# Optimization experiments

Hardware: AMD Instinct MI355X
Metric: run time of the kernel (lower is better)

The kernel has to match this reference:

```python
import jax, jax.numpy as jnp
import numpy as np

NB, D, ED, N, K, DTR = 4, 1024, 2048, 32, 4, 64
B, L = 1, 1024


def setup_inputs():
    key = jax.random.key(0)
    ks = jax.random.split(key, 10)
    g = lambda k, s, sc=0.02: jax.random.normal(k, s, dtype=jnp.float32) * sc
    A_log = jnp.log(jnp.broadcast_to(jnp.arange(1, N + 1, dtype=jnp.float32), (NB, ED, N))) + 0.0
    return {
        "x": g(ks[0], (B, L, D), 1.0),
        "Wi": g(ks[1], (D, D)),
        "bi": jnp.zeros((D,), jnp.float32),
        "ln_g": jnp.ones((NB, D), jnp.float32),
        "ln_b": jnp.zeros((NB, D), jnp.float32),
        "in_w": g(ks[2], (NB, 2 * ED, D)),
        "conv_w": g(ks[3], (NB, ED, 1, K), 0.2),
        "conv_b": jnp.zeros((NB, ED), jnp.float32),
        "xproj_w": g(ks[4], (NB, DTR + 2 * N, ED)),
        "dtproj_w": g(ks[5], (NB, ED, DTR), 0.1),
        "dtproj_b": jnp.full((NB, ED), -4.0, jnp.float32),
        "A_log": A_log,
        "Dp": jnp.ones((NB, ED), jnp.float32),
        "out_w": g(ks[6], (NB, D, ED)),
        "fn_g": jnp.ones((D,), jnp.float32),
        "fn_b": jnp.zeros((D,), jnp.float32),
        "sp_w": g(ks[7], (N, D)),
        "sp_b": jnp.zeros((N,), jnp.float32),
    }


def layernorm(x, g, b, eps=1e-5):
    m = jnp.mean(x, axis=-1, keepdims=True)
    v = jnp.mean(jnp.square(x - m), axis=-1, keepdims=True)
    return (x - m) * jax.lax.rsqrt(v + eps) * g + b


def mamba(u_in, in_w, conv_w, conv_b, xproj_w, dtproj_w, dtproj_b, A_log, Dp, out_w):
    # u_in: (B, L, D)
    xz = u_in @ in_w.T                       # (B, L, 2*ED)
    u, z = jnp.split(xz, 2, axis=-1)         # each (B, L, ED)
    # causal depthwise conv over time
    uc = jnp.swapaxes(u, 1, 2)               # (B, ED, L)
    uc = jax.lax.conv_general_dilated(uc, conv_w, (1,), [(K - 1, 0)], feature_group_count=ED)
    uc = uc + conv_b[None, :, None]
    u = jax.nn.silu(jnp.swapaxes(uc, 1, 2))  # (B, L, ED)
    x_dbl = u @ xproj_w.T                    # (B, L, DTR + 2N)
    dt, Bm, Cm = jnp.split(x_dbl, [DTR, DTR + N], axis=-1)
    delta = jax.nn.softplus(dt @ dtproj_w.T + dtproj_b)  # (B, L, ED)
    A = -jnp.exp(A_log)                                  # (ED, N)
    dA = jnp.exp(delta[..., None] * A)                   # (B, L, ED, N)
    dBu = (delta * u)[..., None] * Bm[:, :, None, :]     # (B, L, ED, N)

    def step(h, inp):
        dA_t, dBu_t, C_t = inp
        h = dA_t * h + dBu_t
        y = jnp.einsum('ben,bn->be', h, C_t)
        return h, y

    h0 = jnp.zeros((u.shape[0], ED, N), u.dtype)
    _, ys = jax.lax.scan(step, h0, (jnp.swapaxes(dA, 0, 1), jnp.swapaxes(dBu, 0, 1), jnp.swapaxes(Cm, 0, 1)))
    y = jnp.swapaxes(ys, 0, 1) + u * Dp      # (B, L, ED)
    y = y * jax.nn.silu(z)
    return y @ out_w.T                       # (B, L, D)


def reference(x, Wi, bi, ln_g, ln_b, in_w, conv_w, conv_b, xproj_w, dtproj_w, dtproj_b, A_log, Dp, out_w, fn_g, fn_b, sp_w, sp_b):
    h = x @ Wi.T + bi
    for i in range(NB):
        normed = layernorm(h, ln_g[i], ln_b[i])
        h = h + mamba(normed, in_w[i], conv_w[i], conv_b[i], xproj_w[i],
                      dtproj_w[i], dtproj_b[i], A_log[i], Dp[i], out_w[i])
    h = layernorm(h, fn_g, fn_b)
    state = jnp.mean(h, axis=1) @ sp_w.T + sp_b   # (B, N)
    return h, state
```

## Files before the change

### kernel.cpp

```cpp
#include <hip/hip_runtime.h>
#include <math.h>

#define D_    1024
#define ED_   2048
#define NST   32
#define KCONV 4
#define DTR_  64
#define L_    1024
#define NB_   4
#define NCH   8
#define CHUNK (L_ / NCH)
#define ZSPL  4
#define XPZ   16

typedef __bf16 bf16_8 __attribute__((ext_vector_type(8)));
typedef __bf16 bf16_4 __attribute__((ext_vector_type(4)));
typedef float  f32x4  __attribute__((ext_vector_type(4)));

__device__ __forceinline__ float softplus_f(float x) {
  return x > 20.f ? x : log1pf(expf(x));
}
__device__ __forceinline__ float silu_f(float x) {
  return x / (1.f + expf(-x));
}

__global__ __launch_bounds__(256) void f2bf_k(
    const float* __restrict__ in, __bf16* __restrict__ out, int n)
{
  const int i = (blockIdx.x * 256 + threadIdx.x) * 8;
  if (i >= n) return;
  const float4 a = *reinterpret_cast<const float4*>(in + i);
  const float4 b = *reinterpret_cast<const float4*>(in + i + 4);
  bf16_8 v;
  v[0]=(__bf16)a.x; v[1]=(__bf16)a.y; v[2]=(__bf16)a.z; v[3]=(__bf16)a.w;
  v[4]=(__bf16)b.x; v[5]=(__bf16)b.y; v[6]=(__bf16)b.z; v[7]=(__bf16)b.w;
  *reinterpret_cast<bf16_8*>(out + i) = v;
}

__global__ __launch_bounds__(256) void gemm_mfma(
    const __bf16* __restrict__ A, int lda,
    const __bf16* __restrict__ W, int ldw,
    const float* __restrict__ bias, float* __restrict__ C, int ldc,
    int K, int flags)
{
  __shared__ __bf16 As[128 * 64];
  __shared__ __bf16 Ws[128 * 64];
  const int tid  = threadIdx.x;
  const int lane = tid & 63;
  const int w    = tid >> 6;
  const int wr   = w >> 1, wc = w & 1;
  const int row0 = blockIdx.y * 128, col0 = blockIdx.x * 128;

  f32x4 acc[4][4] = {};

  for (int k0 = 0; k0 < K; k0 += 64) {
    #pragma unroll
    for (int j = 0; j < 4; ++j) {
      const int inst = w * 4 + j;
      const int row  = inst * 8 + (lane >> 3);
      const int lu   = (lane & 7) ^ (row & 7);
      __builtin_amdgcn_global_load_lds(
          (const __attribute__((address_space(1))) void*)(A + (size_t)(row0 + row) * lda + k0 + lu * 8),
          (__attribute__((address_space(3))) void*)(&As[inst * 512]), 16, 0, 0);
      __builtin_amdgcn_global_load_lds(
          (const __attribute__((address_space(1))) void*)(W + (size_t)(col0 + row) * ldw + k0 + lu * 8),
          (__attribute__((address_space(3))) void*)(&Ws[inst * 512]), 16, 0, 0);
    }
    __syncthreads();
    const int r16 = lane & 15;
    const int uq  = lane >> 4;
    #pragma unroll
    for (int ks = 0; ks < 2; ++ks) {
      bf16_8 af[4], bfr[4];
      #pragma unroll
      for (int m = 0; m < 4; ++m) {
        const int row = wr * 64 + m * 16 + r16;
        const int pu  = (ks * 4 + uq) ^ (row & 7);
        af[m] = *reinterpret_cast<const bf16_8*>(&As[row * 64 + pu * 8]);
      }
      #pragma unroll
      for (int n = 0; n < 4; ++n) {
        const int row = wc * 64 + n * 16 + r16;
        const int pu  = (ks * 4 + uq) ^ (row & 7);
        bfr[n] = *reinterpret_cast<const bf16_8*>(&Ws[row * 64 + pu * 8]);
      }
      #pragma unroll
      for (int m = 0; m < 4; ++m)
        #pragma unroll
        for (int n = 0; n < 4; ++n)
          acc[m][n] = __builtin_amdgcn_mfma_f32_16x16x32_bf16(af[m], bfr[n], acc[m][n], 0, 0, 0);
    }
    __syncthreads();
  }

  const int crow = (lane >> 4) * 4;
  const int ccol = lane & 15;
  #pragma unroll
  for (int m = 0; m < 4; ++m)
    #pragma unroll
    for (int n = 0; n < 4; ++n) {
      const int col = col0 + wc * 64 + n * 16 + ccol;
      const float bv = (flags & 4) ? bias[col] : 0.f;
      #pragma unroll
      for (int r = 0; r < 4; ++r) {
        const int row = row0 + wr * 64 + m * 16 + crow + r;
        float* cp = C + (size_t)row * ldc + col;
        float v = acc[m][n][r] + bv;
        if (flags & 2) v = softplus_f(v);
        if (flags & 1) v += *cp;
        *cp = v;
      }
    }
}

__global__ __launch_bounds__(256) void gemm_mfma_sk(
    const __bf16* __restrict__ A, const __bf16* __restrict__ W,
    float* __restrict__ partials, int M, int N, int K, int Kc)
{
  __shared__ __bf16 As[128 * 64];
  __shared__ __bf16 Ws[128 * 64];
  const int tid  = threadIdx.x;
  const int lane = tid & 63;
  const int w    = tid >> 6;
  const int wr   = w >> 1, wc = w & 1;
  const int row0 = blockIdx.y * 128, col0 = blockIdx.x * 128;
  const int kbase = blockIdx.z * Kc;

  f32x4 acc[4][4] = {};

  for (int k0 = kbase; k0 < kbase + Kc; k0 += 64) {
    #pragma unroll
    for (int j = 0; j < 4; ++j) {
      const int inst = w * 4 + j;
      const int row  = inst * 8 + (lane >> 3);
      const int lu   = (lane & 7) ^ (row & 7);
      __builtin_amdgcn_global_load_lds(
          (const __attribute__((address_space(1))) void*)(A + (size_t)(row0 + row) * K + k0 + lu * 8),
          (__attribute__((address_space(3))) void*)(&As[inst * 512]), 16, 0, 0);
      __builtin_amdgcn_global_load_lds(
          (const __attribute__((address_space(1))) void*)(W + (size_t)(col0 + row) * K + k0 + lu * 8),
          (__attribute__((address_space(3))) void*)(&Ws[inst * 512]), 16, 0, 0);
    }
    __syncthreads();
    const int r16 = lane & 15;
    const int uq  = lane >> 4;
    #pragma unroll
    for (int ks = 0; ks < 2; ++ks) {
      bf16_8 af[4], bfr[4];
      #pragma unroll
      for (int m = 0; m < 4; ++m) {
        const int row = wr * 64 + m * 16 + r16;
        const int pu  = (ks * 4 + uq) ^ (row & 7);
        af[m] = *reinterpret_cast<const bf16_8*>(&As[row * 64 + pu * 8]);
      }
      #pragma unroll
      for (int n = 0; n < 4; ++n) {
        const int row = wc * 64 + n * 16 + r16;
        const int pu  = (ks * 4 + uq) ^ (row & 7);
        bfr[n] = *reinterpret_cast<const bf16_8*>(&Ws[row * 64 + pu * 8]);
      }
      #pragma unroll
      for (int m = 0; m < 4; ++m)
        #pragma unroll
        for (int n = 0; n < 4; ++n)
          acc[m][n] = __builtin_amdgcn_mfma_f32_16x16x32_bf16(af[m], bfr[n], acc[m][n], 0, 0, 0);
    }
    __syncthreads();
  }

  float* base = partials + (size_t)blockIdx.z * M * N;
  const int crow = (lane >> 4) * 4;
  const int ccol = lane & 15;
  #pragma unroll
  for (int m = 0; m < 4; ++m)
    #pragma unroll
    for (int n = 0; n < 4; ++n) {
      const int col = col0 + wc * 64 + n * 16 + ccol;
      #pragma unroll
      for (int r = 0; r < 4; ++r) {
        const int row = row0 + wr * 64 + m * 16 + crow + r;
        base[(size_t)row * N + col] = acc[m][n][r];
      }
    }
}

__global__ __launch_bounds__(256) void mfma_sk_reduce(
    const float* __restrict__ partials, const float* __restrict__ bias,
    float* __restrict__ C, __bf16* __restrict__ Cbf,
    int elems, int ncols, int nz, int flags)
{
  const int i = (blockIdx.x * 256 + threadIdx.x) * 4;
  if (i >= elems) return;
  float4 s = *reinterpret_cast<const float4*>(partials + i);
  for (int z = 1; z < nz; ++z) {
    const float4 p = *reinterpret_cast<const float4*>(partials + (size_t)z * elems + i);
    s.x += p.x; s.y += p.y; s.z += p.z; s.w += p.w;
  }
  if (flags & 4) {
    const float4 bv = *reinterpret_cast<const float4*>(bias + (i % ncols));
    s.x += bv.x; s.y += bv.y; s.z += bv.z; s.w += bv.w;
  }
  if (flags & 1) {
    const float4 ov = *reinterpret_cast<const float4*>(C + i);
    s.x += ov.x; s.y += ov.y; s.z += ov.z; s.w += ov.w;
  }
  *reinterpret_cast<float4*>(C + i) = s;
  if (flags & 8) {
    bf16_4 b;
    b[0]=(__bf16)s.x; b[1]=(__bf16)s.y; b[2]=(__bf16)s.z; b[3]=(__bf16)s.w;
    *reinterpret_cast<bf16_4*>(Cbf + i) = b;
  }
}

__global__ __launch_bounds__(256) void layernorm_k(
    const float* __restrict__ x, const float* __restrict__ g,
    const float* __restrict__ b, float* __restrict__ out)
{
  __shared__ float red[8];
  const int row = blockIdx.x;
  const int tid = threadIdx.x;
  const float* xr = x + (size_t)row * D_;
  float4 v = *reinterpret_cast<const float4*>(xr + tid * 4);
  float s = v.x + v.y + v.z + v.w;
  #pragma unroll
  for (int off = 32; off; off >>= 1) s += __shfl_down(s, off, 64);
  if ((tid & 63) == 0) red[tid >> 6] = s;
  __syncthreads();
  const float m = (red[0] + red[1] + red[2] + red[3]) * (1.f / D_);
  float dx0 = v.x - m, dx1 = v.y - m, dx2 = v.z - m, dx3 = v.w - m;
  float ss = dx0*dx0 + dx1*dx1 + dx2*dx2 + dx3*dx3;
  #pragma unroll
  for (int off = 32; off; off >>= 1) ss += __shfl_down(ss, off, 64);
  if ((tid & 63) == 0) red[4 + (tid >> 6)] = ss;
  __syncthreads();
  const float var = (red[4] + red[5] + red[6] + red[7]) * (1.f / D_);
  const float rs = rsqrtf(var + 1e-5f);
  const int c = tid * 4;
  const float4 gv = *reinterpret_cast<const float4*>(g + c);
  const float4 bv = *reinterpret_cast<const float4*>(b + c);
  float4 o;
  o.x = dx0 * rs * gv.x + bv.x;
  o.y = dx1 * rs * gv.y + bv.y;
  o.z = dx2 * rs * gv.z + bv.z;
  o.w = dx3 * rs * gv.w + bv.w;
  *reinterpret_cast<float4*>(out + (size_t)row * D_ + c) = o;
}

__global__ __launch_bounds__(256) void layernorm_bf_k(
    const float* __restrict__ x, const float* __restrict__ g,
    const float* __restrict__ b, __bf16* __restrict__ out)
{
  __shared__ float red[8];
  const int row = blockIdx.x;
  const int tid = threadIdx.x;
  const float* xr = x + (size_t)row * D_;
  float4 v = *reinterpret_cast<const float4*>(xr + tid * 4);
  float s = v.x + v.y + v.z + v.w;
  #pragma unroll
  for (int off = 32; off; off >>= 1) s += __shfl_down(s, off, 64);
  if ((tid & 63) == 0) red[tid >> 6] = s;
  __syncthreads();
  const float m = (red[0] + red[1] + red[2] + red[3]) * (1.f / D_);
  float dx0 = v.x - m, dx1 = v.y - m, dx2 = v.z - m, dx3 = v.w - m;
  float ss = dx0*dx0 + dx1*dx1 + dx2*dx2 + dx3*dx3;
  #pragma unroll
  for (int off = 32; off; off >>= 1) ss += __shfl_down(ss, off, 64);
  if ((tid & 63) == 0) red[4 + (tid >> 6)] = ss;
  __syncthreads();
  const float var = (red[4] + red[5] + red[6] + red[7]) * (1.f / D_);
  const float rs = rsqrtf(var + 1e-5f);
  const int c = tid * 4;
  const float4 gv = *reinterpret_cast<const float4*>(g + c);
  const float4 bv = *reinterpret_cast<const float4*>(b + c);
  bf16_4 o;
  o[0] = (__bf16)(dx0 * rs * gv.x + bv.x);
  o[1] = (__bf16)(dx1 * rs * gv.y + bv.y);
  o[2] = (__bf16)(dx2 * rs * gv.z + bv.z);
  o[3] = (__bf16)(dx3 * rs * gv.w + bv.w);
  *reinterpret_cast<bf16_4*>(out + (size_t)row * D_ + c) = o;
}

__global__ __launch_bounds__(256) void conv_silu_k(
    const float* __restrict__ xz, const float* __restrict__ cw,
    const float* __restrict__ cb, float* __restrict__ u, __bf16* __restrict__ ub)
{
  const int e = blockIdx.x * 256 + threadIdx.x;
  const int t0 = blockIdx.y * 8;
  const float w0 = cw[e*4+0], w1 = cw[e*4+1], w2 = cw[e*4+2], w3 = cw[e*4+3];
  const float b = cb[e];
  float x0 = (t0 >= 3) ? xz[(size_t)(t0-3)*(2*ED_)+e] : 0.f;
  float x1 = (t0 >= 2) ? xz[(size_t)(t0-2)*(2*ED_)+e] : 0.f;
  float x2 = (t0 >= 1) ? xz[(size_t)(t0-1)*(2*ED_)+e] : 0.f;
  #pragma unroll
  for (int j = 0; j < 8; ++j) {
    const float x3 = xz[(size_t)(t0+j)*(2*ED_)+e];
    const float uv = silu_f(b + w0*x0 + w1*x1 + w2*x2 + w3*x3);
    u[(size_t)(t0+j)*ED_+e] = uv;
    ub[(size_t)(t0+j)*ED_+e] = (__bf16)uv;
    x0 = x1; x1 = x2; x2 = x3;
  }
}

__global__ __launch_bounds__(256) void scan_phase1(
    const float* __restrict__ delta, const float* __restrict__ u,
    const float* __restrict__ xdbl, const float* __restrict__ A_log,
    float* __restrict__ hend, float* __restrict__ Pend)
{
  __shared__ float dl[16][8], ul[16][8];
  __shared__ float bl[16][32];
  const int tid = threadIdx.x;
  const int n = tid & 31;
  const int c = tid >> 5;
  const int e0 = blockIdx.x * 8;
  const int e = e0 + c;
  const int ch = blockIdx.y;
  const float a = -expf(A_log[e * NST + n]);
  float h = 0.f, S = 0.f;
  const int t0 = ch * CHUNK;
  const int s_t = (tid & 127) >> 3, s_e = tid & 7;
  const int b_c = (tid & 7) * 4;

  float rg_a = 0.f;
  float4 rg_b;
  if (tid < 128) {
    rg_a = delta[(size_t)(t0 + s_t) * ED_ + e0 + s_e];
    rg_b = *reinterpret_cast<const float4*>(&xdbl[(size_t)(t0 + s_t) * 128 + 64 + b_c]);
  } else {
    rg_a = u[(size_t)(t0 + s_t) * ED_ + e0 + s_e];
  }

  for (int tb = 0; tb < CHUNK; tb += 16) {
    if (tid < 128) {
      dl[s_t][s_e] = rg_a;
      *reinterpret_cast<float4*>(&bl[s_t][b_c]) = rg_b;
    } else {
      ul[s_t][s_e] = rg_a;
    }
    __syncthreads();
    if (tb + 16 < CHUNK) {
      const int t = t0 + tb + 16 + s_t;
      if (tid < 128) {
        rg_a = delta[(size_t)t * ED_ + e0 + s_e];
        rg_b = *reinterpret_cast<const float4*>(&xdbl[(size_t)t * 128 + 64 + b_c]);
      } else {
        rg_a = u[(size_t)t * ED_ + e0 + s_e];
      }
    }
    #pragma unroll
    for (int j = 0; j < 16; ++j) {
      const float sd = dl[j][c];
      const float uv = ul[j][c];
      const float Bv = bl[j][n];
      h = fmaf(__expf(sd * a), h, sd * uv * Bv);
      S += sd;
    }
    __syncthreads();
  }
  const int idx = ch * (ED_ * NST) + blockIdx.x * 256 + tid;
  hend[idx] = h;
  Pend[idx] = __expf(a * S);
}

__global__ __launch_bounds__(256, 7) void scan_phase3(
    const float* __restrict__ delta, const float* __restrict__ u,
    const float* __restrict__ xdbl, const float* __restrict__ A_log,
    const float* __restrict__ hend, const float* __restrict__ Pend,
    const float* __restrict__ Dp,
    const float* __restrict__ xz, __bf16* __restrict__ y)
{
  __shared__ float p_lds[8][16][33];
  __shared__ float dl[16][8], ul[16][8], zl[16][8];
  __shared__ float bc[16][64];
  const int tid = threadIdx.x;
  const int n = tid & 31;
  const int c = tid >> 5;
  const int e0 = blockIdx.x * 8;
  const int e = e0 + c;
  const int ch = blockIdx.y;
  const float a = -expf(A_log[e * NST + n]);
  const float dp = Dp[e];

  float h = 0.f;
  {
    const int sidx = blockIdx.x * 256 + tid;
    for (int cc = 0; cc < ch; ++cc) {
      const int off = cc * (ED_ * NST) + sidx;
      h = fmaf(Pend[off], h, hend[off]);
    }
  }

  const int t0 = ch * CHUNK;
  const int r = n & 15, half = n >> 4;
  const int s_t  = (tid & 127) >> 3;
  const int s_e  = tid & 7;
  const int b_t  = tid >> 4;
  const int b_c  = (tid & 15) * 4;

  float rg_a = 0.f, rg_z = 0.f;
  float4 rg_bc;
  {
    const int t = t0 + s_t;
    if (tid < 128) {
      rg_a = delta[(size_t)t * ED_ + e0 + s_e];
      rg_z = xz[(size_t)t * (2*ED_) + ED_ + e0 + s_e];
    } else {
      rg_a = u[(size_t)t * ED_ + e0 + s_e];
    }
    rg_bc = *reinterpret_cast<const float4*>(&xdbl[(size_t)(t0 + b_t) * 128 + 64 + b_c]);
  }

  for (int tb = 0; tb < CHUNK; tb += 16) {
    if (tid < 128) { dl[s_t][s_e] = rg_a; zl[s_t][s_e] = rg_z; }
    else          { ul[s_t][s_e] = rg_a; }
    *reinterpret_cast<float4*>(&bc[b_t][b_c]) = rg_bc;
    __syncthreads();
    if (tb + 16 < CHUNK) {
      const int t = t0 + tb + 16 + s_t;
      if (tid < 128) {
        rg_a = delta[(size_t)t * ED_ + e0 + s_e];
        rg_z = xz[(size_t)t * (2*ED_) + ED_ + e0 + s_e];
      } else {
        rg_a = u[(size_t)t * ED_ + e0 + s_e];
      }
      rg_bc = *reinterpret_cast<const float4*>(&xdbl[(size_t)(t0 + tb + 16 + b_t) * 128 + 64 + b_c]);
    }
    #pragma unroll
    for (int j = 0; j < 16; ++j) {
      const float sd = dl[j][c];
      const float uv = ul[j][c];
      const float Bv = bc[j][n];
      const float Cv = bc[j][32 + n];
      const float dA = __expf(sd * a);
      h = fmaf(dA, h, sd * uv * Bv);
      p_lds[c][j][n] = h * Cv;
    }
    __syncthreads();
    float s = 0.f;
    #pragma unroll
    for (int k = 0; k < 16; ++k) s += p_lds[c][r][half * 16 + k];
    s += __shfl_xor(s, 16, 64);
    if (half == 0) {
      const float uvt = ul[r][c];
      const float zv  = zl[r][c];
      y[(size_t)(t0 + tb + r) * ED_ + e] = (__bf16)((s + uvt * dp) * silu_f(zv));
    }
    __syncthreads();
  }
}

__global__ __launch_bounds__(256) void colmean_part_k(
    const float* __restrict__ hf, float* __restrict__ part)
{
  const int d = blockIdx.x * 256 + threadIdx.x;
  const int tc = blockIdx.y;
  float s = 0.f;
  #pragma unroll 8
  for (int j = 0; j < 32; ++j) s += hf[(size_t)(tc * 32 + j) * D_ + d];
  part[tc * D_ + d] = s;
}

__global__ __launch_bounds__(256) void colmean_fin_k(
    const float* __restrict__ part, float* __restrict__ cm)
{
  const int d = blockIdx.x * 256 + threadIdx.x;
  float s = 0.f;
  #pragma unroll
  for (int c = 0; c < 32; ++c) s += part[c * D_ + d];
  cm[d] = s * (1.f / L_);
}

__global__ __launch_bounds__(256) void state_k(
    const float* __restrict__ cm, const float* __restrict__ spw,
    const float* __restrict__ spb, float* __restrict__ out)
{
  __shared__ float red[4];
  const int nidx = blockIdx.x;
  const int tid = threadIdx.x;
  float s = 0.f;
  for (int d = tid; d < D_; d += 256) s += cm[d] * spw[(size_t)nidx * D_ + d];
  #pragma unroll
  for (int off = 32; off; off >>= 1) s += __shfl_down(s, off, 64);
  if ((tid & 63) == 0) red[tid >> 6] = s;
  __syncthreads();
  if (tid == 0) out[nidx] = red[0] + red[1] + red[2] + red[3] + spb[nidx];
}

extern "C" void kernel_launch(void* const* d_in, const int* in_sizes, int n_in,
                              void* d_out, int out_size, void* d_ws, size_t ws_size,
                              hipStream_t stream) {
  const float* x        = (const float*)d_in[0];
  const float* Wi       = (const float*)d_in[1];
  const float* bi       = (const float*)d_in[2];
  const float* ln_g     = (const float*)d_in[3];
  const float* ln_b     = (const float*)d_in[4];
  const float* in_w     = (const float*)d_in[5];
  const float* conv_w   = (const float*)d_in[6];
  const float* conv_b   = (const float*)d_in[7];
  const float* xproj_w  = (const float*)d_in[8];
  const float* dtproj_w = (const float*)d_in[9];
  const float* dtproj_b = (const float*)d_in[10];
  const float* A_log    = (const float*)d_in[11];
  const float* Dp       = (const float*)d_in[12];
  const float* out_w    = (const float*)d_in[13];
  const float* fn_g     = (const float*)d_in[14];
  const float* fn_b     = (const float*)d_in[15];
  const float* sp_w     = (const float*)d_in[16];
  const float* sp_b     = (const float*)d_in[17];
  float* out  = (float*)d_out;
  float* ws_f = (float*)d_ws;

  float* h_buf  = ws_f;
  float* xz     = ws_f + 1048576;
  float* u_buf  = ws_f + 5242880;
  float* xdbl   = ws_f + 7340032;
  float* delta  = ws_f + 7471104;
  float* hend   = ws_f + 9568256;
  float* pend   = ws_f + 10092544;
  float* cmean  = ws_f + 10616832;
  __bf16* nbf   = (__bf16*)(ws_f + 10617856);
  __bf16* ybf   = (__bf16*)(ws_f + 11142144);
  __bf16* wbf   = (__bf16*)(ws_f + 12190720);
  __bf16* xdblbf= (__bf16*)(ws_f + 16385024);
  __bf16* dtwbf = (__bf16*)(ws_f + 16450560);
  __bf16* ubf   = (__bf16*)(ws_f + 16516096);
  __bf16* xpbf  = (__bf16*)(ws_f + 17564672);
  float* skmf   = u_buf;
  float* skxp   = delta;
  float* cmpart = hend;

  const dim3 blk(256);

  f2bf_k<<<512, blk, 0, stream>>>(x, nbf, L_ * D_);
  f2bf_k<<<512, blk, 0, stream>>>(Wi, wbf, D_ * D_);
  gemm_mfma_sk<<<dim3(D_/128, L_/128, ZSPL), blk, 0, stream>>>(
      nbf, wbf, skmf, L_, D_, D_, D_/ZSPL);
  mfma_sk_reduce<<<dim3(L_*D_/4/256), blk, 0, stream>>>(
      skmf, bi, h_buf, nullptr, L_*D_, D_, ZSPL, 4);

  for (int i = 0; i < NB_; ++i) {
    layernorm_bf_k<<<L_, blk, 0, stream>>>(h_buf, ln_g + i*D_, ln_b + i*D_, nbf);
    f2bf_k<<<2048, blk, 0, stream>>>(in_w + (size_t)i*2*ED_*D_, wbf, 2*ED_*D_);
    gemm_mfma<<<dim3(2*ED_/128, L_/128), blk, 0, stream>>>(
        nbf, D_, wbf, D_, nullptr, xz, 2*ED_, D_, 0);
    conv_silu_k<<<dim3(ED_/256, L_/8), blk, 0, stream>>>(
        xz, conv_w + (size_t)i*ED_*KCONV, conv_b + (size_t)i*ED_, u_buf, ubf);
    f2bf_k<<<128, blk, 0, stream>>>(xproj_w + (size_t)i*128*ED_, xpbf, 128*ED_);
    gemm_mfma_sk<<<dim3(1, L_/128, XPZ), blk, 0, stream>>>(
        ubf, xpbf, skxp, L_, 128, ED_, ED_/XPZ);
    mfma_sk_reduce<<<dim3(L_*128/4/256), blk, 0, stream>>>(
        skxp, nullptr, xdbl, xdblbf, L_*128, 128, XPZ, 8);
    f2bf_k<<<64, blk, 0, stream>>>(dtproj_w + (size_t)i*ED_*DTR_, dtwbf, ED_*DTR_);
    gemm_mfma<<<dim3(ED_/128, L_/128), blk, 0, stream>>>(
        xdblbf, 128, dtwbf, DTR_, dtproj_b + (size_t)i*ED_, delta, ED_, DTR_, 2 | 4);
    scan_phase1<<<dim3(ED_/8, NCH), blk, 0, stream>>>(
        delta, u_buf, xdbl, A_log + (size_t)i*ED_*NST, hend, pend);
    scan_phase3<<<dim3(ED_/8, NCH), blk, 0, stream>>>(
        delta, u_buf, xdbl, A_log + (size_t)i*ED_*NST, hend, pend,
        Dp + (size_t)i*ED_, xz, ybf);
    f2bf_k<<<1024, blk, 0, stream>>>(out_w + (size_t)i*D_*ED_, wbf, D_*ED_);
    gemm_mfma_sk<<<dim3(D_/128, L_/128, ZSPL), blk, 0, stream>>>(
        ybf, wbf, skmf, L_, D_, ED_, ED_/ZSPL);
    mfma_sk_reduce<<<dim3(L_*D_/4/256), blk, 0, stream>>>(
        skmf, nullptr, h_buf, nullptr, L_*D_, D_, ZSPL, 1);
  }

  layernorm_k<<<L_, blk, 0, stream>>>(h_buf, fn_g, fn_b, out);
  colmean_part_k<<<dim3(D_/256, 32), blk, 0, stream>>>(out, cmpart);
  colmean_fin_k<<<D_/256, blk, 0, stream>>>(cmpart, cmean);
  state_k<<<NST, blk, 0, stream>>>(cmean, sp_w, sp_b, out + (size_t)L_*D_);
}
```

Baseline: 673.6 us.

## Batch weight conversions, add XCD block swizzle, fuse colmean finish into state

Combines the four per-block fp32-to-bf16 weight conversions into one multi-segment kernel launched at the start of each layer, and gives out_w its own bf16 buffer. Adds an XCD-aware workgroup remap in both GEMM kernels so neighbouring tiles share an L2. Folds the colmean finish step into the state projection kernel. The aim is fewer launches and better cache locality, at the cost of extra workspace and a branchy conversion kernel; the swizzle assumes the workgroup count is divisible by 8.

```diff
diff --git a/kernel.cpp b/kernel.cpp
--- a/kernel.cpp
+++ b/kernel.cpp
@@ -24,11 +24,26 @@
   return x / (1.f + expf(-x));
 }
 
-__global__ __launch_bounds__(256) void f2bf_k(
-    const float* __restrict__ in, __bf16* __restrict__ out, int n)
-{
-  const int i = (blockIdx.x * 256 + threadIdx.x) * 8;
-  if (i >= n) return;
+__device__ __forceinline__ int xcd_swz(int lin, int nwg) {
+  const int q = nwg >> 3;
+  return (lin & 7) * q + (lin >> 3);
+}
+
+__global__ __launch_bounds__(256) void f2bf4_k(
+    const float* __restrict__ i0, __bf16* __restrict__ o0, int n0,
+    const float* __restrict__ i1, __bf16* __restrict__ o1, int n1,
+    const float* __restrict__ i2, __bf16* __restrict__ o2, int n2,
+    const float* __restrict__ i3, __bf16* __restrict__ o3, int n3)
+{
+  int gid = blockIdx.x * 256 + threadIdx.x;
+  const int u0 = n0 >> 3, u1 = n1 >> 3, u2 = n2 >> 3, u3 = n3 >> 3;
+  const float* in; __bf16* out;
+  if (gid < u0) { in = i0; out = o0; }
+  else if ((gid -= u0) < u1) { in = i1; out = o1; }
+  else if ((gid -= u1) < u2) { in = i2; out = o2; }
+  else if ((gid -= u2) < u3) { in = i3; out = o3; }
+  else return;
+  const int i = gid * 8;
   const float4 a = *reinterpret_cast<const float4*>(in + i);
   const float4 b = *reinterpret_cast<const float4*>(in + i + 4);
   bf16_8 v;
@@ -49,7 +64,10 @@
   const int lane = tid & 63;
   const int w    = tid >> 6;
   const int wr   = w >> 1, wc = w & 1;
-  const int row0 = blockIdx.y * 128, col0 = blockIdx.x * 128;
+  const int nwg  = gridDim.x * gridDim.y;
+  const int swz  = xcd_swz(blockIdx.y * gridDim.x + blockIdx.x, nwg);
+  const int bx   = swz % gridDim.x, by = swz / gridDim.x;
+  const int row0 = by * 128, col0 = bx * 128;
 
   f32x4 acc[4][4] = {};
 
@@ -123,8 +141,14 @@
   const int lane = tid & 63;
   const int w    = tid >> 6;
   const int wr   = w >> 1, wc = w & 1;
-  const int row0 = blockIdx.y * 128, col0 = blockIdx.x * 128;
-  const int kbase = blockIdx.z * Kc;
+  const int nwg  = gridDim.x * gridDim.y * gridDim.z;
+  const int lin  = (blockIdx.z * gridDim.y + blockIdx.y) * gridDim.x + blockIdx.x;
+  const int swz  = xcd_swz(lin, nwg);
+  const int bx   = swz % gridDim.x;
+  const int tmp  = swz / gridDim.x;
+  const int by   = tmp % gridDim.y, bz = tmp / gridDim.y;
+  const int row0 = by * 128, col0 = bx * 128;
+  const int kbase = bz * Kc;
 
   f32x4 acc[4][4] = {};
 
@@ -168,7 +192,7 @@
     __syncthreads();
   }
 
-  float* base = partials + (size_t)blockIdx.z * M * N;
+  float* base = partials + (size_t)bz * M * N;
   const int crow = (lane >> 4) * 4;
   const int ccol = lane & 15;
   #pragma unroll
@@ -459,25 +483,20 @@
   part[tc * D_ + d] = s;
 }
 
-__global__ __launch_bounds__(256) void colmean_fin_k(
-    const float* __restrict__ part, float* __restrict__ cm)
-{
-  const int d = blockIdx.x * 256 + threadIdx.x;
-  float s = 0.f;
-  #pragma unroll
-  for (int c = 0; c < 32; ++c) s += part[c * D_ + d];
-  cm[d] = s * (1.f / L_);
-}
-
-__global__ __launch_bounds__(256) void state_k(
-    const float* __restrict__ cm, const float* __restrict__ spw,
+__global__ __launch_bounds__(256) void state_fused_k(
+    const float* __restrict__ part, const float* __restrict__ spw,
     const float* __restrict__ spb, float* __restrict__ out)
 {
   __shared__ float red[4];
   const int nidx = blockIdx.x;
   const int tid = threadIdx.x;
   float s = 0.f;
-  for (int d = tid; d < D_; d += 256) s += cm[d] * spw[(size_t)nidx * D_ + d];
+  for (int d = tid; d < D_; d += 256) {
+    float cm = 0.f;
+    #pragma unroll
+    for (int c = 0; c < 32; ++c) cm += part[c * D_ + d];
+    s += cm * (1.f / L_) * spw[(size_t)nidx * D_ + d];
+  }
   #pragma unroll
   for (int off = 32; off; off >>= 1) s += __shfl_down(s, off, 64);
   if ((tid & 63) == 0) red[tid >> 6] = s;
@@ -516,7 +535,6 @@
   float* delta  = ws_f + 7471104;
   float* hend   = ws_f + 9568256;
   float* pend   = ws_f + 10092544;
-  float* cmean  = ws_f + 10616832;
   __bf16* nbf   = (__bf16*)(ws_f + 10617856);
   __bf16* ybf   = (__bf16*)(ws_f + 11142144);
   __bf16* wbf   = (__bf16*)(ws_f + 12190720);
@@ -524,32 +542,35 @@
   __bf16* dtwbf = (__bf16*)(ws_f + 16450560);
   __bf16* ubf   = (__bf16*)(ws_f + 16516096);
   __bf16* xpbf  = (__bf16*)(ws_f + 17564672);
+  __bf16* owbf  = (__bf16*)(ws_f + 17695744);
   float* skmf   = u_buf;
   float* skxp   = delta;
   float* cmpart = hend;
 
   const dim3 blk(256);
 
-  f2bf_k<<<512, blk, 0, stream>>>(x, nbf, L_ * D_);
-  f2bf_k<<<512, blk, 0, stream>>>(Wi, wbf, D_ * D_);
+  f2bf4_k<<<1024, blk, 0, stream>>>(x, nbf, L_*D_, Wi, wbf, D_*D_,
+                                    x, nbf, 0, x, nbf, 0);
   gemm_mfma_sk<<<dim3(D_/128, L_/128, ZSPL), blk, 0, stream>>>(
       nbf, wbf, skmf, L_, D_, D_, D_/ZSPL);
   mfma_sk_reduce<<<dim3(L_*D_/4/256), blk, 0, stream>>>(
       skmf, bi, h_buf, nullptr, L_*D_, D_, ZSPL, 4);
 
   for (int i = 0; i < NB_; ++i) {
+    f2bf4_k<<<3264, blk, 0, stream>>>(
+        in_w    + (size_t)i*2*ED_*D_, wbf,   2*ED_*D_,
+        xproj_w + (size_t)i*128*ED_,  xpbf,  128*ED_,
+        dtproj_w+ (size_t)i*ED_*DTR_, dtwbf, ED_*DTR_,
+        out_w   + (size_t)i*D_*ED_,   owbf,  D_*ED_);
     layernorm_bf_k<<<L_, blk, 0, stream>>>(h_buf, ln_g + i*D_, ln_b + i*D_, nbf);
-    f2bf_k<<<2048, blk, 0, stream>>>(in_w + (size_t)i*2*ED_*D_, wbf, 2*ED_*D_);
     gemm_mfma<<<dim3(2*ED_/128, L_/128), blk, 0, stream>>>(
         nbf, D_, wbf, D_, nullptr, xz, 2*ED_, D_, 0);
     conv_silu_k<<<dim3(ED_/256, L_/8), blk, 0, stream>>>(
         xz, conv_w + (size_t)i*ED_*KCONV, conv_b + (size_t)i*ED_, u_buf, ubf);
-    f2bf_k<<<128, blk, 0, stream>>>(xproj_w + (size_t)i*128*ED_, xpbf, 128*ED_);
     gemm_mfma_sk<<<dim3(1, L_/128, XPZ), blk, 0, stream>>>(
         ubf, xpbf, skxp, L_, 128, ED_, ED_/XPZ);
     mfma_sk_reduce<<<dim3(L_*128/4/256), blk, 0, stream>>>(
         skxp, nullptr, xdbl, xdblbf, L_*128, 128, XPZ, 8);
-    f2bf_k<<<64, blk, 0, stream>>>(dtproj_w + (size_t)i*ED_*DTR_, dtwbf, ED_*DTR_);
     gemm_mfma<<<dim3(ED_/128, L_/128), blk, 0, stream>>>(
         xdblbf, 128, dtwbf, DTR_, dtproj_b + (size_t)i*ED_, delta, ED_, DTR_, 2 | 4);
     scan_phase1<<<dim3(ED_/8, NCH), blk, 0, stream>>>(
@@ -557,15 +578,13 @@
     scan_phase3<<<dim3(ED_/8, NCH), blk, 0, stream>>>(
         delta, u_buf, xdbl, A_log + (size_t)i*ED_*NST, hend, pend,
         Dp + (size_t)i*ED_, xz, ybf);
-    f2bf_k<<<1024, blk, 0, stream>>>(out_w + (size_t)i*D_*ED_, wbf, D_*ED_);
     gemm_mfma_sk<<<dim3(D_/128, L_/128, ZSPL), blk, 0, stream>>>(
-        ybf, wbf, skmf, L_, D_, ED_, ED_/ZSPL);
+        ybf, owbf, skmf, L_, D_, ED_, ED_/ZSPL);
     mfma_sk_reduce<<<dim3(L_*D_/4/256), blk, 0, stream>>>(
         skmf, nullptr, h_buf, nullptr, L_*D_, D_, ZSPL, 1);
   }
 
   layernorm_k<<<L_, blk, 0, stream>>>(h_buf, fn_g, fn_b, out);
   colmean_part_k<<<dim3(D_/256, 32), blk, 0, stream>>>(out, cmpart);
-  colmean_fin_k<<<D_/256, blk, 0, stream>>>(cmpart, cmean);
-  state_k<<<NST, blk, 0, stream>>>(cmean, sp_w, sp_b, out + (size_t)L_*D_);
-}
+  state_fused_k<<<NST, blk, 0, stream>>>(cmpart, sp_w, sp_b, out + (size_t)L_*D_);
+}
```

Result: faster. 650.4 us (-3.4%).
